# Performance work log

Hardware: AMD Instinct MI355X
Metric: run time of the kernel (lower is better)

## Reference

```python
import jax, jax.numpy as jnp
import numpy as np

N, S, E = 8, 2048, 512
H, D = 8, 64            # heads, head_dim
P = 16                  # num_persistent
ALIBI_ALPHA = 1.0
START_I = 0


def setup_inputs() -> dict:
    key = jax.random.key(0)
    ks = jax.random.split(key, 12)
    inp = {
        "values": jax.random.normal(ks[0], (N, S, E), jnp.float32),
        "keys": jax.random.normal(ks[1], (N, S, E), jnp.float32),
        "queries": jax.random.normal(ks[2], (N, S, E), jnp.float32),
        "mask": jax.random.randint(ks[3], (N, 1, S, S), 0, 2, jnp.int32),
        # per-head-dim projections (torch Linear, no bias): weight shape (out, in)
        "Wv": jax.random.normal(ks[4], (D, D), jnp.float32) / np.sqrt(D),
        "Wk": jax.random.normal(ks[5], (D, D), jnp.float32) / np.sqrt(D),
        "Wq": jax.random.normal(ks[6], (D, D), jnp.float32) / np.sqrt(D),
        "Wo": jax.random.normal(ks[7], (E, E), jnp.float32) / np.sqrt(E),
        "bo": jnp.zeros((E,), jnp.float32),
        # talking-heads 1x1 conv weights, squeezed to (H_out, H_in)
        "pre_th": jax.random.normal(ks[8], (H, H), jnp.float32) / np.sqrt(H),
        "post_th": jax.random.normal(ks[9], (H, H), jnp.float32) / np.sqrt(H),
        # persistent memory tokens (P, H, D)
        "pk": jax.random.normal(ks[10], (P, H, D), jnp.float32) * 0.1,
        "pv": jax.random.normal(ks[11], (P, H, D), jnp.float32) * 0.1,
    }
    return inp


def reference(values, keys, queries, mask, Wv, Wk, Wq, Wo, bo, pre_th, post_th, pk, pv):
    n, q_len, e = queries.shape
    k_len = keys.shape[1]
    h, d = pk.shape[1], pk.shape[2]

    # split heads: [n, s, h, d]
    v = values.reshape(n, -1, h, d)
    k = keys.reshape(n, -1, h, d)
    q = queries.reshape(n, -1, h, d)

    # per-head-dim linear projections (torch: x @ W.T)
    v = jnp.einsum('nshd,ed->nshe', v, Wv)
    k = jnp.einsum('nshd,ed->nshe', k, Wk)
    q = jnp.einsum('nshd,ed->nshe', q, Wq)

    # append persistent memory tokens along key/value sequence dim
    p = pk.shape[0]
    k = jnp.concatenate([k, jnp.broadcast_to(pk[None], (n, p, h, d))], axis=1)
    v = jnp.concatenate([v, jnp.broadcast_to(pv[None], (n, p, h, d))], axis=1)

    # energy: [n, h, q, k_len + p]
    energy = jnp.einsum('nqhd,nkhd->nhqk', q, k)

    # ALiBi bias: -|i - j| * slope_h, zero bias on persistent slots
    slopes = 2.0 ** (-ALIBI_ALPHA * (jnp.arange(1, h + 1, dtype=jnp.float32) + START_I))
    t_q = jnp.arange(q_len)
    t_k = jnp.arange(k_len)
    dist = jnp.abs(t_q[:, None] - t_k[None, :]).astype(jnp.float32)  # [q, k]
    alibi = -dist[None, None] * slopes[None, :, None, None]          # [1, h, q, k]
    alibi = jnp.pad(alibi, ((0, 0), (0, 0), (0, 0), (0, p)))
    energy = energy + alibi

    # pre-softmax talking heads (1x1 conv over head channel)
    energy = jnp.einsum('ij,njqk->niqk', pre_th, energy)

    # mask (pad persistent slots with 1 = keep)
    mask_p = jnp.pad(mask, ((0, 0), (0, 0), (0, 0), (0, p)), constant_values=1)
    energy = jnp.where(mask_p == 0, jnp.float32(-1e4), energy)

    attn = jax.nn.softmax(energy / jnp.sqrt(jnp.float32(e)), axis=3)

    # post-softmax talking heads
    attn = jnp.einsum('ij,njqk->niqk', post_th, attn)

    out = jnp.einsum('nhql,nlhd->nqhd', attn, v).reshape(n, q_len, e)
    out = out @ Wo.T + bo
    return out
```

## Files before the change

### kernel.cpp

```cpp
#include <hip/hip_runtime.h>

#define N_ 8
#define S_ 2048
#define E_ 512
#define KL_ 2064
#define NTT_ 65
#define VTSZ 1064960
#define SCALE2 0.063758723f
#define NEGBIG -700.0f

typedef unsigned short u16;
typedef unsigned int u32;
typedef __attribute__((ext_vector_type(2))) float f32x2;
typedef __attribute__((ext_vector_type(4))) float f32x4;
typedef __attribute__((ext_vector_type(4))) short bf16x4;
typedef __attribute__((ext_vector_type(8))) short bf16x8;

__device__ __forceinline__ u16 f2bf(float x) {
  u32 u = __float_as_uint(x);
  u32 r = (u + 0x7FFFu + ((u >> 16) & 1u)) >> 16;
  return (u16)r;
}

__device__ __forceinline__ float exp2_fast(float x) {
  float r;
  asm("v_exp_f32 %0, %1" : "=v"(r) : "v"(x));
  return r;
}

__device__ __forceinline__ f32x4 mfma16(bf16x4 a, bf16x4 b, f32x4 c) {
#if __has_builtin(__builtin_amdgcn_mfma_f32_16x16x16bf16_1k)
  return __builtin_amdgcn_mfma_f32_16x16x16bf16_1k(a, b, c, 0, 0, 0);
#else
  f32x4 d;
  asm("v_mfma_f32_16x16x16_bf16 %0, %1, %2, %3" : "=v"(d) : "v"(a), "v"(b), "v"(c));
  return d;
#endif
}

__device__ __forceinline__ void gload_lds16(const void* g, void* l) {
  __builtin_amdgcn_global_load_lds((const __attribute__((address_space(1))) unsigned int*)g,
                                   (__attribute__((address_space(3))) unsigned int*)l, 16, 0, 0);
}

__global__ __launch_bounds__(256) void maskpack_kernel(const int* __restrict__ mask,
                                                       u32* __restrict__ bm) {
  const int t = threadIdx.x;
  const int w = t >> 6, lane = t & 63;
  const int blk = blockIdx.x;
  const int n = blk >> 9;
  const int qrow = ((blk & 511) << 2) + w;
  const int* row = mask + ((size_t)n * S_ + qrow) * S_;
  __shared__ u32 tl[4][64];
  u32 myword = 0;
  #pragma unroll 4
  for (int k = 0; k < 32; ++k) {
    int v = row[k * 64 + lane];
    unsigned long long b = __ballot(v != 0);
    if ((lane >> 1) == k) myword = (lane & 1) ? (u32)(b >> 32) : (u32)b;
  }
  tl[w][lane] = myword;
  __syncthreads();
  const int qq = t & 3, wi = t >> 2;
  const int qb = ((blk & 511) << 2) + qq;
  bm[((size_t)n * 64 + wi) * S_ + qb] = tl[qq][wi];
}

__global__ __launch_bounds__(256, 2) void proj_kernel(
    const float* __restrict__ V_, const float* __restrict__ K_, const float* __restrict__ Q_,
    const float* __restrict__ Wv, const float* __restrict__ Wk, const float* __restrict__ Wq,
    u16* __restrict__ Kp, u16* __restrict__ Qp, u16* __restrict__ VT) {
  __shared__ u16 xt[64 * 512];
  __shared__ u16 wt[64 * 64];
  const int tz = blockIdx.y;
  const float* X = (tz == 0) ? V_ : (tz == 1) ? K_ : Q_;
  const float* W = (tz == 0) ? Wv : (tz == 1) ? Wk : Wq;
  const int t = threadIdx.x, lane = t & 63, w = t >> 6, g = lane >> 4, li = lane & 15;
  const int rb = blockIdx.x * 64;
  const int nn = rb >> 11, sb = rb & 2047;

  for (int c = t; c < 512; c += 256) {
    int r = c >> 3, s = c & 7;
    float4 a = *(const float4*)&W[r * 64 + s * 8];
    float4 b = *(const float4*)&W[r * 64 + s * 8 + 4];
    bf16x8 v = {(short)f2bf(a.x), (short)f2bf(a.y), (short)f2bf(a.z), (short)f2bf(a.w),
                (short)f2bf(b.x), (short)f2bf(b.y), (short)f2bf(b.z), (short)f2bf(b.w)};
    *(bf16x8*)&wt[r * 64 + ((s ^ (r & 7)) * 8)] = v;
  }
  for (int c = t; c < 4096; c += 256) {
    int r = c >> 6, s = c & 63;
    const float* src = &X[(size_t)(rb + r) * 512 + s * 8];
    float4 a = *(const float4*)src;
    float4 b = *(const float4*)(src + 4);
    bf16x8 v = {(short)f2bf(a.x), (short)f2bf(a.y), (short)f2bf(a.z), (short)f2bf(a.w),
                (short)f2bf(b.x), (short)f2bf(b.y), (short)f2bf(b.z), (short)f2bf(b.w)};
    *(bf16x8*)&xt[r * 512 + ((s ^ (r & 7)) * 8)] = v;
  }
  __syncthreads();

  bf16x8 fx[8][2];
  #pragma unroll
  for (int h = 0; h < 8; ++h)
    #pragma unroll
    for (int dh = 0; dh < 2; ++dh) {
      int row = w * 16 + li;
      fx[h][dh] = *(const bf16x8*)&xt[row * 512 + (((h * 8 + dh * 4 + g) ^ (row & 7)) * 8)];
    }
  bf16x8 fw[4][2];
  #pragma unroll
  for (int c = 0; c < 4; ++c)
    #pragma unroll
    for (int dh = 0; dh < 2; ++dh) {
      int row = c * 16 + li;
      fw[c][dh] = *(const bf16x8*)&wt[row * 64 + (((dh * 4 + g) ^ (row & 7)) * 8)];
    }

  f32x4 C[8][4];
  #pragma unroll
  for (int h = 0; h < 8; ++h)
    #pragma unroll
    for (int c = 0; c < 4; ++c) C[h][c] = (f32x4){0.f, 0.f, 0.f, 0.f};

  if (tz == 0) {
    #pragma unroll
    for (int h = 0; h < 8; ++h)
      #pragma unroll
      for (int dh = 0; dh < 2; ++dh)
        #pragma unroll
        for (int c = 0; c < 4; ++c)
          C[h][c] = __builtin_amdgcn_mfma_f32_16x16x32_bf16(fw[c][dh], fx[h][dh], C[h][c], 0, 0, 0);
    #pragma unroll
    for (int h = 0; h < 8; ++h)
      #pragma unroll
      for (int c = 0; c < 4; ++c)
        #pragma unroll
        for (int r = 0; r < 4; ++r) {
          int e = h * 64 + c * 16 + g * 4 + r;
          int l = sb + w * 16 + li;
          VT[(((size_t)nn * 65 + (l >> 5)) * 512 + e) * 32 + (l & 31)] = f2bf(C[h][c][r]);
        }
  } else {
    #pragma unroll
    for (int h = 0; h < 8; ++h)
      #pragma unroll
      for (int dh = 0; dh < 2; ++dh)
        #pragma unroll
        for (int c = 0; c < 4; ++c)
          C[h][c] = __builtin_amdgcn_mfma_f32_16x16x32_bf16(fx[h][dh], fw[c][dh], C[h][c], 0, 0, 0);
    #pragma unroll
    for (int h = 0; h < 8; ++h)
      #pragma unroll
      for (int c = 0; c < 4; ++c)
        #pragma unroll
        for (int r = 0; r < 4; ++r) {
          int e = h * 64 + c * 16 + li;
          u16 val = f2bf(C[h][c][r]);
          if (tz == 2) Qp[(size_t)(rb + w * 16 + g * 4 + r) * 512 + e] = val;
          else Kp[((size_t)nn * KL_ + sb + w * 16 + g * 4 + r) * 512 + e] = val;
        }
  }
}

__global__ __launch_bounds__(256) void persist_kernel(const float* __restrict__ pk,
                                                      const float* __restrict__ pv,
                                                      u16* __restrict__ Kp, u16* __restrict__ VT) {
  int id = blockIdx.x * 256 + threadIdx.x;
  if (id < 65536) {
    int n = id >> 13, p = (id >> 9) & 15, e = id & 511;
    Kp[((size_t)n * KL_ + S_ + p) * 512 + e] = f2bf(pk[p * 512 + e]);
  } else {
    int rem = id - 65536;
    int n = rem >> 14, p = (rem >> 9) & 31, e = rem & 511;
    u16 val = (p < 16) ? f2bf(pv[p * 512 + e]) : (u16)0;
    VT[(((size_t)n * 65 + 64) * 512 + e) * 32 + p] = val;
  }
}

__global__ __launch_bounds__(512, 4) void z_kernel(
    const u16* __restrict__ Qp, const u16* __restrict__ Kp,
    const u32* __restrict__ bm, const float* __restrict__ pre_th,
    float* __restrict__ Zp) {
  __shared__ __align__(16) u16 KtB[2][32 * 512];
  __shared__ u32 mlds[33 * 64];
  __shared__ float Zbuf[2 * 64 * 8];

  const int t = threadIdx.x, lane = t & 63, w = t >> 6, g = lane >> 4, li = lane & 15;
  const int qw = w & 3, lh = w >> 2;
  const int bid = blockIdx.x;
  const int n = bid & 7;
  const int rem = bid >> 3;
  const int qb = rem >> 1, kh = rem & 1;
  const int q0 = qb * 64;
  const int tb = kh ? 33 : 0;
  const int nt = kh ? 32 : 33;
  const int wc = kh ? 31 : 33;
  const int myq = q0 + qw * 16 + li;
  const float myq_f = (float)myq;

  const u16* Kbase = Kp + (size_t)n * KL_ * 512;

  #define ZSTAGE_K(buf, tile) {                                                         \
    _Pragma("unroll")                                                                   \
    for (int i_ = 0; i_ < 4; ++i_) {                                                    \
      int row_ = w + i_ * 8;                                                            \
      gload_lds16(Kbase + (size_t)((tile) * 32 + row_) * 512 + ((lane ^ (row_ & 7)) * 8),\
                  &KtB[buf][row_ * 512]);                                               \
    } }

  for (int idx = t; idx < wc * 64; idx += 512)
    mlds[idx] = bm[((size_t)n * 64 + tb + (idx >> 6)) * S_ + q0 + (idx & 63)];

  bf16x8 qf[8][2];
  {
    const u16* qrow = Qp + (size_t)(n * S_ + myq) * 512;
    #pragma unroll
    for (int h = 0; h < 8; ++h)
      #pragma unroll
      for (int dh = 0; dh < 2; ++dh)
        qf[h][dh] = *(const bf16x8*)(qrow + h * 64 + dh * 32 + g * 8);
  }
  float nms[8];
  #pragma unroll
  for (int i = 0; i < 8; ++i) {
    float a = 0.f;
    #pragma unroll
    for (int j = 0; j < 8; ++j) a += pre_th[i * 8 + j] * exp2f(-(float)(j + 1));
    nms[i] = -a * SCALE2;
  }

  float Zr[8];
  #pragma unroll
  for (int i = 0; i < 8; ++i) Zr[i] = 0.f;

  ZSTAGE_K(0, tb)
  __syncthreads();

  for (int j = 0; j < nt; ++j) {
    const int tile = tb + j;
    if (j + 1 < nt) ZSTAGE_K((j + 1) & 1, tb + j + 1)
    __builtin_amdgcn_sched_barrier(0);
    const u16* kb = &KtB[j & 1][0];
    f32x4 C[8];
    #pragma unroll
    for (int h = 0; h < 8; ++h) C[h] = (f32x4){0.f, 0.f, 0.f, 0.f};
    #pragma unroll
    for (int h = 0; h < 8; ++h)
      #pragma unroll
      for (int dh = 0; dh < 2; ++dh) {
        bf16x8 a = *(const bf16x8*)(kb + (lh * 16 + li) * 512 + (((h * 8 + dh * 4 + g) ^ (li & 7)) * 8));
        C[h] = __builtin_amdgcn_mfma_f32_16x16x32_bf16(a, qf[h][dh], C[h], 0, 0, 0);
      }
    u32 mbits;
    float dist[4];
    const int l0 = tile * 32 + lh * 16 + g * 4;
    if (tile < 64) {
      mbits = (mlds[j * 64 + qw * 16 + li] >> (lh * 16 + g * 4)) & 0xFu;
      #pragma unroll
      for (int r = 0; r < 4; ++r) dist[r] = fabsf(myq_f - (float)(l0 + r));
    } else {
      mbits = (lh == 0) ? 0xFu : 0u;
      #pragma unroll
      for (int r = 0; r < 4; ++r) dist[r] = 0.f;
    }
    const bool al = (tile < 64);
    #pragma unroll
    for (int i = 0; i < 8; ++i) {
      f32x2 al2 = (f32x2){0.f, 0.f}, ah2 = (f32x2){0.f, 0.f};
      #pragma unroll
      for (int j2 = 0; j2 < 8; ++j2) {
        float p = pre_th[i * 8 + j2];
        al2 += p * (f32x2){C[j2].x, C[j2].y};
        ah2 += p * (f32x2){C[j2].z, C[j2].w};
      }
      float t0 = fmaf(al2.x, SCALE2, -64.f);
      float t1 = fmaf(al2.y, SCALE2, -64.f);
      float t2 = fmaf(ah2.x, SCALE2, -64.f);
      float t3 = fmaf(ah2.y, SCALE2, -64.f);
      if (al) {
        t0 = fmaf(dist[0], nms[i], t0); t1 = fmaf(dist[1], nms[i], t1);
        t2 = fmaf(dist[2], nms[i], t2); t3 = fmaf(dist[3], nms[i], t3);
      }
      t0 = (mbits & 1u) ? t0 : NEGBIG; t1 = (mbits & 2u) ? t1 : NEGBIG;
      t2 = (mbits & 4u) ? t2 : NEGBIG; t3 = (mbits & 8u) ? t3 : NEGBIG;
      Zr[i] += (exp2_fast(t0) + exp2_fast(t1)) + (exp2_fast(t2) + exp2_fast(t3));
    }
    asm volatile("s_waitcnt vmcnt(0)" ::: "memory");
    __builtin_amdgcn_s_barrier();
  }

  #pragma unroll
  for (int i = 0; i < 8; ++i) {
    Zr[i] += __shfl_xor(Zr[i], 16);
    Zr[i] += __shfl_xor(Zr[i], 32);
  }
  if (lane < 16) {
    #pragma unroll
    for (int i = 0; i < 8; ++i) Zbuf[(lh * 64 + qw * 16 + li) * 8 + i] = Zr[i];
  }
  __syncthreads();
  {
    int q = t >> 3, i = t & 7;
    float val = Zbuf[q * 8 + i] + Zbuf[(64 + q) * 8 + i];
    Zp[((size_t)(kh * 8 + n) * 2048 + q0 + q) * 8 + i] = val;
  }
  #undef ZSTAGE_K
}

__global__ __launch_bounds__(512, 2) void pv_kernel(
    const u16* __restrict__ Qp, const u16* __restrict__ Kp, const u16* __restrict__ VT,
    const u32* __restrict__ bm, const float* __restrict__ pre_th,
    const float* __restrict__ post_th, const float* __restrict__ Zp,
    u16* __restrict__ Ohb) {
  __shared__ __align__(16) char smem[151552];
  u16* KtB = (u16*)smem;
  u16* VtB = (u16*)(smem + 65536);
  u32* mlds = (u32*)(smem + 131072);

  const int t = threadIdx.x, lane = t & 63, w = t >> 6, g = lane >> 4, li = lane & 15;
  const int qw = w & 3, lh = w >> 2;
  const int bid = blockIdx.x;
  const int n = bid & 7;
  const int q0 = (bid >> 3) * 64;
  const int myq = q0 + qw * 16 + li;
  const float myq_f = (float)myq;

  const u16* Kbase = Kp + (size_t)n * KL_ * 512;
  const u16* Vbase = VT + (size_t)n * VTSZ;

  #define STAGE_K(buf, tile) {                                                          \
    _Pragma("unroll")                                                                   \
    for (int i_ = 0; i_ < 4; ++i_) {                                                    \
      int row_ = w + i_ * 8;                                                            \
      gload_lds16(Kbase + (size_t)((tile) * 32 + row_) * 512 + ((lane ^ (row_ & 7)) * 8),\
                  KtB + (buf) * 16384 + row_ * 512);                                    \
    } }
  #define STAGE_V(buf, tile) {                                                          \
    _Pragma("unroll")                                                                   \
    for (int i_ = 0; i_ < 4; ++i_) {                                                    \
      int c_ = t + i_ * 512;                                                            \
      int e_ = c_ >> 2, q16_ = c_ & 3;                                                  \
      gload_lds16(Vbase + (size_t)(tile) * 16384 + e_ * 32 + ((q16_ ^ (e_ & 3)) * 8),   \
                  VtB + (buf) * 16384 + (i_ * 512 + w * 64) * 8);                       \
    } }

  for (int idx = t; idx < 4096; idx += 512)
    mlds[idx] = bm[((size_t)n * 64 + (idx >> 6)) * S_ + q0 + (idx & 63)];

  bf16x8 qf[8][2];
  {
    const u16* qrow = Qp + (size_t)(n * S_ + myq) * 512;
    #pragma unroll
    for (int h = 0; h < 8; ++h)
      #pragma unroll
      for (int dh = 0; dh < 2; ++dh)
        qf[h][dh] = *(const bf16x8*)(qrow + h * 64 + dh * 32 + g * 8);
  }
  float nms[8];
  #pragma unroll
  for (int i = 0; i < 8; ++i) {
    float a = 0.f;
    #pragma unroll
    for (int j = 0; j < 8; ++j) a += pre_th[i * 8 + j] * exp2f(-(float)(j + 1));
    nms[i] = -a * SCALE2;
  }
  float nm1[8];
  {
    const float* zp0 = Zp + ((size_t)n * 2048 + myq) * 8;
    const float* zp1 = Zp + ((size_t)(8 + n) * 2048 + myq) * 8;
    #pragma unroll
    for (int i = 0; i < 8; ++i) nm1[i] = -(64.f + __log2f(zp0[i] + zp1[i]));
  }

  f32x4 O[8][4];
  #pragma unroll
  for (int o = 0; o < 8; ++o)
    #pragma unroll
    for (int dc = 0; dc < 4; ++dc) O[o][dc] = (f32x4){0.f, 0.f, 0.f, 0.f};

  const int cloff = (((lh * 2 + (g >> 1)) ^ (li & 3)) * 8) + (g & 1) * 4;

  STAGE_K(0, 0)
  STAGE_V(0, 0)
  __syncthreads();

  for (int tt = 0; tt < NTT_; ++tt) {
    if (tt + 1 < NTT_) { STAGE_K((tt + 1) & 1, tt + 1) STAGE_V((tt + 1) & 1, tt + 1) }
    __builtin_amdgcn_sched_barrier(0);
    const u16* kb = KtB + (tt & 1) * 16384;
    const u16* vb = VtB + (tt & 1) * 16384;
    f32x4 C[8];
    #pragma unroll
    for (int h = 0; h < 8; ++h) C[h] = (f32x4){0.f, 0.f, 0.f, 0.f};
    #pragma unroll
    for (int h = 0; h < 8; ++h)
      #pragma unroll
      for (int dh = 0; dh < 2; ++dh) {
        bf16x8 a = *(const bf16x8*)(kb + (lh * 16 + li) * 512 + (((h * 8 + dh * 4 + g) ^ (li & 7)) * 8));
        C[h] = __builtin_amdgcn_mfma_f32_16x16x32_bf16(a, qf[h][dh], C[h], 0, 0, 0);
      }
    u32 mbits;
    float dist[4];
    const int l0 = tt * 32 + lh * 16 + g * 4;
    if (tt < 64) {
      mbits = (mlds[tt * 64 + qw * 16 + li] >> (lh * 16 + g * 4)) & 0xFu;
      #pragma unroll
      for (int r = 0; r < 4; ++r) dist[r] = fabsf(myq_f - (float)(l0 + r));
    } else {
      mbits = (lh == 0) ? 0xFu : 0u;
      #pragma unroll
      for (int r = 0; r < 4; ++r) dist[r] = 0.f;
    }
    f32x2 accl[8], acch[8];
    #pragma unroll
    for (int i = 0; i < 8; ++i) { accl[i] = (f32x2){0.f, 0.f}; acch[i] = (f32x2){0.f, 0.f}; }
    #pragma unroll
    for (int j = 0; j < 8; ++j) {
      f32x2 elo = {C[j].x, C[j].y}, ehi = {C[j].z, C[j].w};
      #pragma unroll
      for (int i = 0; i < 8; ++i) {
        float p = pre_th[i * 8 + j];
        accl[i] += p * elo; acch[i] += p * ehi;
      }
    }
    const bool al = (tt < 64);
    f32x2 ppl[8], pph[8];
    #pragma unroll
    for (int i = 0; i < 8; ++i) {
      float t0 = fmaf(accl[i].x, SCALE2, nm1[i]);
      float t1 = fmaf(accl[i].y, SCALE2, nm1[i]);
      float t2 = fmaf(acch[i].x, SCALE2, nm1[i]);
      float t3 = fmaf(acch[i].y, SCALE2, nm1[i]);
      if (al) {
        t0 = fmaf(dist[0], nms[i], t0); t1 = fmaf(dist[1], nms[i], t1);
        t2 = fmaf(dist[2], nms[i], t2); t3 = fmaf(dist[3], nms[i], t3);
      }
      t0 = (mbits & 1u) ? t0 : NEGBIG; t1 = (mbits & 2u) ? t1 : NEGBIG;
      t2 = (mbits & 4u) ? t2 : NEGBIG; t3 = (mbits & 8u) ? t3 : NEGBIG;
      ppl[i] = (f32x2){exp2_fast(t0), exp2_fast(t1)};
      pph[i] = (f32x2){exp2_fast(t2), exp2_fast(t3)};
    }
    f32x2 pol[8], poh[8];
    #pragma unroll
    for (int o = 0; o < 8; ++o) { pol[o] = (f32x2){0.f, 0.f}; poh[o] = (f32x2){0.f, 0.f}; }
    #pragma unroll
    for (int i = 0; i < 8; ++i) {
      #pragma unroll
      for (int o = 0; o < 8; ++o) {
        float c = post_th[o * 8 + i];
        pol[o] += c * ppl[i]; poh[o] += c * pph[i];
      }
    }
    #pragma unroll
    for (int o = 0; o < 8; ++o) {
      bf16x4 pa = {(short)f2bf(pol[o].x), (short)f2bf(pol[o].y),
                   (short)f2bf(poh[o].x), (short)f2bf(poh[o].y)};
      #pragma unroll
      for (int dc = 0; dc < 4; ++dc) {
        int e = o * 64 + dc * 16 + li;
        bf16x4 b = *(const bf16x4*)(vb + e * 32 + cloff);
        O[o][dc] = mfma16(pa, b, O[o][dc]);
      }
    }
    asm volatile("s_waitcnt vmcnt(0)" ::: "memory");
    __builtin_amdgcn_s_barrier();
  }

  float* ep = (float*)smem;
  if (lh == 1) {
    #pragma unroll
    for (int o = 0; o < 8; ++o)
      #pragma unroll
      for (int dc = 0; dc < 4; ++dc)
        *(f32x4*)&ep[qw * 8192 + ((o * 4 + dc) * 64 + li * 4 + g) * 4] = O[o][dc];
  }
  __syncthreads();
  if (lh == 0) {
    u16* dst = Ohb + (size_t)(n * S_ + q0 + qw * 16) * 512;
    #pragma unroll
    for (int o = 0; o < 8; ++o)
      #pragma unroll
      for (int dc = 0; dc < 4; ++dc) {
        f32x4 oth = *(const f32x4*)&ep[qw * 8192 + ((o * 4 + dc) * 64 + li * 4 + g) * 4];
        f32x4 v = O[o][dc] + oth;
        int e = o * 64 + dc * 16 + li;
        #pragma unroll
        for (int r = 0; r < 4; ++r) dst[(size_t)(g * 4 + r) * 512 + e] = f2bf(v[r]);
      }
  }
  #undef STAGE_K
  #undef STAGE_V
}

__global__ __launch_bounds__(256) void out_proj_kernel(
    const u16* __restrict__ Ohb, const float* __restrict__ Wo,
    const float* __restrict__ bo, float* __restrict__ out) {
  __shared__ __align__(16) u16 As[2][128 * 32];
  __shared__ __align__(16) u16 Bs[2][128 * 32];
  const int t = threadIdx.x, lane = t & 63, w = t >> 6, g = lane >> 4, li = lane & 15;
  const int wq = w & 1, wp = w >> 1;
  const int r0 = blockIdx.y * 128, c0 = blockIdx.x * 128;

  #define STAGE_A(buf, ks) {                                                  \
    _Pragma("unroll")                                                         \
    for (int i_ = 0; i_ < 2; ++i_) {                                          \
      int c_ = t + i_ * 256;                                                  \
      gload_lds16(Ohb + (size_t)(r0 + (c_ >> 2)) * 512 + (ks) + (c_ & 3) * 8, \
                  &As[buf][(i_ * 256 + w * 64) * 8]);                         \
    } }
  #define STAGE_B(buf, ks) {                                                  \
    _Pragma("unroll")                                                         \
    for (int i_ = 0; i_ < 2; ++i_) {                                          \
      int c_ = t + i_ * 256;                                                  \
      const float* s_ = &Wo[(size_t)(c0 + (c_ >> 2)) * 512 + (ks) + (c_ & 3) * 8]; \
      float4 a_ = *(const float4*)s_;                                         \
      float4 b_ = *(const float4*)(s_ + 4);                                   \
      bf16x8 v_ = {(short)f2bf(a_.x), (short)f2bf(a_.y), (short)f2bf(a_.z), (short)f2bf(a_.w), \
                   (short)f2bf(b_.x), (short)f2bf(b_.y), (short)f2bf(b_.z), (short)f2bf(b_.w)}; \
      *(bf16x8*)&Bs[buf][c_ * 8] = v_;                                        \
    } }

  f32x4 acc[4][4];
  #pragma unroll
  for (int m = 0; m < 4; ++m)
    #pragma unroll
    for (int nn = 0; nn < 4; ++nn) acc[m][nn] = (f32x4){0.f, 0.f, 0.f, 0.f};

  STAGE_A(0, 0)
  STAGE_B(0, 0)
  __syncthreads();
  for (int s = 0; s < 16; ++s) {
    if (s + 1 < 16) { STAGE_A((s + 1) & 1, (s + 1) * 32) STAGE_B((s + 1) & 1, (s + 1) * 32) }
    const u16* ab = As[s & 1];
    const u16* bb = Bs[s & 1];
    bf16x8 af[4], bf[4];
    #pragma unroll
    for (int m = 0; m < 4; ++m) af[m] = *(const bf16x8*)(ab + (wp * 64 + m * 16 + li) * 32 + g * 8);
    #pragma unroll
    for (int nn = 0; nn < 4; ++nn) bf[nn] = *(const bf16x8*)(bb + (wq * 64 + nn * 16 + li) * 32 + g * 8);
    #pragma unroll
    for (int m = 0; m < 4; ++m)
      #pragma unroll
      for (int nn = 0; nn < 4; ++nn)
        acc[m][nn] = __builtin_amdgcn_mfma_f32_16x16x32_bf16(af[m], bf[nn], acc[m][nn], 0, 0, 0);
    __syncthreads();
  }
  #pragma unroll
  for (int nn = 0; nn < 4; ++nn) {
    int col = c0 + wq * 64 + nn * 16 + li;
    float bv = bo[col];
    #pragma unroll
    for (int m = 0; m < 4; ++m)
      #pragma unroll
      for (int r = 0; r < 4; ++r)
        out[(size_t)(r0 + wp * 64 + m * 16 + g * 4 + r) * 512 + col] = acc[m][nn][r] + bv;
  }
  #undef STAGE_A
  #undef STAGE_B
}

extern "C" void kernel_launch(void* const* d_in, const int* in_sizes, int n_in,
                              void* d_out, int out_size, void* d_ws, size_t ws_size,
                              hipStream_t stream) {
  const float* values  = (const float*)d_in[0];
  const float* keys    = (const float*)d_in[1];
  const float* queries = (const float*)d_in[2];
  const int*   mask    = (const int*)d_in[3];
  const float* Wv      = (const float*)d_in[4];
  const float* Wk      = (const float*)d_in[5];
  const float* Wq      = (const float*)d_in[6];
  const float* Wo      = (const float*)d_in[7];
  const float* bo      = (const float*)d_in[8];
  const float* pre_th  = (const float*)d_in[9];
  const float* post_th = (const float*)d_in[10];
  const float* pk      = (const float*)d_in[11];
  const float* pv      = (const float*)d_in[12];

  char* ws = (char*)d_ws;
  u16*  Qp  = (u16*)ws;
  u16*  Kp  = (u16*)(ws + 16777216);
  u16*  VT  = (u16*)(ws + 33685504);
  u16*  Ohb = (u16*)(ws + 50724864);
  u32*  bm  = (u32*)(ws + 67502080);
  float* Zp = (float*)(ws + 71696384);

  hipLaunchKernelGGL(maskpack_kernel, dim3(4096), dim3(256), 0, stream, mask, bm);
  hipLaunchKernelGGL(proj_kernel, dim3(256, 3), dim3(256), 0, stream,
                     values, keys, queries, Wv, Wk, Wq, Kp, Qp, VT);
  hipLaunchKernelGGL(persist_kernel, dim3(768), dim3(256), 0, stream, pk, pv, Kp, VT);
  hipLaunchKernelGGL(z_kernel, dim3(512), dim3(512), 0, stream,
                     Qp, Kp, bm, pre_th, Zp);
  hipLaunchKernelGGL(pv_kernel, dim3(256), dim3(512), 0, stream,
                     Qp, Kp, VT, bm, pre_th, post_th, Zp, Ohb);
  hipLaunchKernelGGL(out_proj_kernel, dim3(4, 128), dim3(256), 0, stream,
                     Ohb, Wo, bo, (float*)d_out);
}
```

Measured before the change: 971.6 us.

## Replace double-buffered K/V staging with single-buffered load-then-compute loop

Removes the ping-pong LDS buffers for K and V tiles in both z_kernel and pv_kernel. Each iteration now loads the current tile, waits for it, runs a barrier, computes, then barriers again before the next load. This halves the tile LDS footprint, though the declared shared arrays in pv_kernel keep their size. The cost is that global-to-LDS loads no longer overlap with the MFMA and softmax work, so every tile exposes its load latency.

New measurement: 939.0 us. 1.03x faster.

```diff
diff --git a/kernel.cpp b/kernel.cpp
--- a/kernel.cpp
+++ b/kernel.cpp
@@ -180,7 +180,7 @@
     const u16* __restrict__ Qp, const u16* __restrict__ Kp,
     const u32* __restrict__ bm, const float* __restrict__ pre_th,
     float* __restrict__ Zp) {
-  __shared__ __align__(16) u16 KtB[2][32 * 512];
+  __shared__ __align__(16) u16 KtB[32 * 512];
   __shared__ u32 mlds[33 * 64];
   __shared__ float Zbuf[2 * 64 * 8];
 
@@ -199,12 +199,12 @@
 
   const u16* Kbase = Kp + (size_t)n * KL_ * 512;
 
-  #define ZSTAGE_K(buf, tile) {                                                         \
+  #define ZSTAGE_K(tile) {                                                              \
     _Pragma("unroll")                                                                   \
     for (int i_ = 0; i_ < 4; ++i_) {                                                    \
       int row_ = w + i_ * 8;                                                            \
       gload_lds16(Kbase + (size_t)((tile) * 32 + row_) * 512 + ((lane ^ (row_ & 7)) * 8),\
-                  &KtB[buf][row_ * 512]);                                               \
+                  &KtB[row_ * 512]);                                                    \
     } }
 
   for (int idx = t; idx < wc * 64; idx += 512)
@@ -232,14 +232,15 @@
   #pragma unroll
   for (int i = 0; i < 8; ++i) Zr[i] = 0.f;
 
-  ZSTAGE_K(0, tb)
   __syncthreads();
 
   for (int j = 0; j < nt; ++j) {
     const int tile = tb + j;
-    if (j + 1 < nt) ZSTAGE_K((j + 1) & 1, tb + j + 1)
+    ZSTAGE_K(tile)
     __builtin_amdgcn_sched_barrier(0);
-    const u16* kb = &KtB[j & 1][0];
+    asm volatile("s_waitcnt vmcnt(0)" ::: "memory");
+    __builtin_amdgcn_s_barrier();
+    const u16* kb = &KtB[0];
     f32x4 C[8];
     #pragma unroll
     for (int h = 0; h < 8; ++h) C[h] = (f32x4){0.f, 0.f, 0.f, 0.f};
@@ -284,9 +285,9 @@
       t2 = (mbits & 4u) ? t2 : NEGBIG; t3 = (mbits & 8u) ? t3 : NEGBIG;
       Zr[i] += (exp2_fast(t0) + exp2_fast(t1)) + (exp2_fast(t2) + exp2_fast(t3));
     }
-    asm volatile("s_waitcnt vmcnt(0)" ::: "memory");
     __builtin_amdgcn_s_barrier();
   }
+  __syncthreads();
 
   #pragma unroll
   for (int i = 0; i < 8; ++i) {
@@ -313,7 +314,7 @@
     u16* __restrict__ Ohb) {
   __shared__ __align__(16) char smem[151552];
   u16* KtB = (u16*)smem;
-  u16* VtB = (u16*)(smem + 65536);
+  u16* VtB = (u16*)(smem + 32768);
   u32* mlds = (u32*)(smem + 131072);
 
   const int t = threadIdx.x, lane = t & 63, w = t >> 6, g = lane >> 4, li = lane & 15;
@@ -327,20 +328,20 @@
   const u16* Kbase = Kp + (size_t)n * KL_ * 512;
   const u16* Vbase = VT + (size_t)n * VTSZ;
 
-  #define STAGE_K(buf, tile) {                                                          \
+  #define STAGE_K(tile) {                                                               \
     _Pragma("unroll")                                                                   \
     for (int i_ = 0; i_ < 4; ++i_) {                                                    \
       int row_ = w + i_ * 8;                                                            \
       gload_lds16(Kbase + (size_t)((tile) * 32 + row_) * 512 + ((lane ^ (row_ & 7)) * 8),\
-                  KtB + (buf) * 16384 + row_ * 512);                                    \
+                  KtB + row_ * 512);                                                    \
     } }
-  #define STAGE_V(buf, tile) {                                                          \
+  #define STAGE_V(tile) {                                                               \
     _Pragma("unroll")                                                                   \
     for (int i_ = 0; i_ < 4; ++i_) {                                                    \
       int c_ = t + i_ * 512;                                                            \
       int e_ = c_ >> 2, q16_ = c_ & 3;                                                  \
       gload_lds16(Vbase + (size_t)(tile) * 16384 + e_ * 32 + ((q16_ ^ (e_ & 3)) * 8),   \
-                  VtB + (buf) * 16384 + (i_ * 512 + w * 64) * 8);                       \
+                  VtB + (i_ * 512 + w * 64) * 8);                                       \
     } }
 
   for (int idx = t; idx < 4096; idx += 512)
@@ -379,15 +380,15 @@
 
   const int cloff = (((lh * 2 + (g >> 1)) ^ (li & 3)) * 8) + (g & 1) * 4;
 
-  STAGE_K(0, 0)
-  STAGE_V(0, 0)
   __syncthreads();
 
   for (int tt = 0; tt < NTT_; ++tt) {
-    if (tt + 1 < NTT_) { STAGE_K((tt + 1) & 1, tt + 1) STAGE_V((tt + 1) & 1, tt + 1) }
+    STAGE_K(tt) STAGE_V(tt)
     __builtin_amdgcn_sched_barrier(0);
-    const u16* kb = KtB + (tt & 1) * 16384;
-    const u16* vb = VtB + (tt & 1) * 16384;
+    asm volatile("s_waitcnt vmcnt(0)" ::: "memory");
+    __builtin_amdgcn_s_barrier();
+    const u16* kb = KtB;
+    const u16* vb = VtB;
     f32x4 C[8];
     #pragma unroll
     for (int h = 0; h < 8; ++h) C[h] = (f32x4){0.f, 0.f, 0.f, 0.f};
@@ -461,9 +462,9 @@
         O[o][dc] = mfma16(pa, b, O[o][dc]);
       }
     }
-    asm volatile("s_waitcnt vmcnt(0)" ::: "memory");
     __builtin_amdgcn_s_barrier();
   }
+  __syncthreads();
 
   float* ep = (float*)smem;
   if (lh == 1) {
```
